# Kernel optimization log

Hardware: AMD Instinct MI355X
Metric: run time of the kernel (lower is better)

Reference implementation:

```python
import jax, jax.numpy as jnp
import numpy as np

TWO_PI = 2.0 * np.pi


def setup_inputs() -> dict:
    key = jax.random.key(0)
    k1, k2, k3, k4 = jax.random.split(key, 4)
    N, H, W, B = 1024, 256, 256, 64
    pred = jax.random.uniform(k1, (N,), dtype=jnp.float32)
    mu = jax.random.uniform(k2, (N, 2), dtype=jnp.float32)              # centers in [0,1]
    sigma = jax.random.uniform(k3, (N, 2), dtype=jnp.float32) * 0.25 + 0.05  # widths in [0.05,0.30]
    nodes = jnp.concatenate([mu, sigma], axis=1)                         # [N,4]
    batch_list = jax.random.randint(k4, (N,), 0, B, dtype=jnp.int64)
    return {"pred": pred, "nodes": nodes, "batch_list": batch_list,
            "h": H, "w": W, "batch_num": B}


def reference(pred, nodes, batch_list, h, w, batch_num):
    # Normalized grid, identical to torch.arange(num)*step + start
    xs = jnp.linspace(0.0, 1.0, w, dtype=pred.dtype)   # [w]
    ys = jnp.linspace(0.0, 1.0, h, dtype=pred.dtype)   # [h]
    x_t = xs[None, :]                                   # broadcasts to [h,w]
    y_t = ys[:, None]

    mu_x = nodes[:, 0][:, None, None]
    mu_y = nodes[:, 1][:, None, None]
    sx = nodes[:, 2][:, None, None]
    sy = nodes[:, 3][:, None, None]

    # [N,h,w] per-node gaussian (epsilon = 0 in the original module)
    g = (1.0 / (TWO_PI * sx * sy)) * jnp.exp(
        -((x_t[None] - mu_x) ** 2 / (2.0 * sx ** 2)
          + (y_t[None] - mu_y) ** 2 / (2.0 * sy ** 2)))

    # normalize each node map by its max, scale by pred[i]
    g = g / jnp.max(g, axis=(1, 2), keepdims=True) * pred[:, None, None]

    # scatter-add into per-batch maps
    maps = jax.ops.segment_sum(g, batch_list, num_segments=batch_num)   # [B,h,w]
    return maps[:, None, :, :]                                          # [B,1,h,w]
```

## Files before the change

### kernel.cpp

```cpp
#include <hip/hip_runtime.h>
#include <math.h>

#define HCONST 256
#define WCONST 256
#define ROWS   32
#define TILES  (HCONST / ROWS)
#define CHUNK  64

__global__ __launch_bounds__(256) void fused_kernel(
    const float* __restrict__ pred,
    const float* __restrict__ nodes,
    const int*   __restrict__ batch_list,
    int N,
    float* __restrict__ out)
{
    const int b  = blockIdx.x / TILES;
    const int ty = blockIdx.x % TILES;
    const int y0 = ty * ROWS;
    const int t  = threadIdx.x;
    const int xi   = t & 127;
    const int half = t >> 7;

    __shared__ int    s_idx[1024];
    __shared__ int    s_cnt;
    __shared__ float4 s_prm[CHUNK];
    __shared__ float  s_fy[CHUNK][ROWS];

    if (t == 0) s_cnt = 0;
    __syncthreads();
    for (int n = t; n < N; n += 256) {
        if (batch_list[n] == b) {
            int p = atomicAdd(&s_cnt, 1);
            s_idx[p] = n;
        }
    }
    __syncthreads();
    const int cnt = s_cnt;

    const float step = 1.0f / 255.0f;
    const float x0s = (2 * xi)     * step;
    const float x1s = (2 * xi + 1) * step;

    float2 acc[16];
#pragma unroll
    for (int r = 0; r < 16; ++r) acc[r] = make_float2(0.0f, 0.0f);

    for (int c0 = 0; c0 < cnt; c0 += CHUNK) {
        const int cc = min(CHUNK, cnt - c0);

        for (int p = t; p < cc; p += 256) {
            const int n = s_idx[c0 + p];
            const float4 nd = ((const float4*)nodes)[n];
            const float ax = 1.0f / (2.0f * nd.z * nd.z);
            float ni = roundf(nd.x * 255.0f);
            ni = fminf(fmaxf(ni, 0.0f), 255.0f);
            const float dxm = ni * step - nd.x;
            s_prm[p] = make_float4(nd.x, ax, ax * dxm * dxm, 0.0f);
        }
        for (int it = t; it < cc * ROWS; it += 256) {
            const int g  = it >> 5;
            const int yy = it & 31;
            const int n  = s_idx[c0 + g];
            const float4 nd = ((const float4*)nodes)[n];
            const float ay = 1.0f / (2.0f * nd.w * nd.w);
            float ni = roundf(nd.y * 255.0f);
            ni = fminf(fmaxf(ni, 0.0f), 255.0f);
            const float dym = ni * step - nd.y;
            const float dy  = (y0 + yy) * step - nd.y;
            s_fy[g][yy] = pred[n] * __expf(ay * (dym * dym - dy * dy));
        }
        __syncthreads();

        for (int g = 0; g < cc; ++g) {
            const float4 prm = s_prm[g];
            const float dx0 = x0s - prm.x;
            const float dx1 = x1s - prm.x;
            const float e0 = __expf(prm.z - prm.y * dx0 * dx0);
            const float e1 = __expf(prm.z - prm.y * dx1 * dx1);
            const float4* fy4 = (const float4*)&s_fy[g][half * 16];
#pragma unroll
            for (int k = 0; k < 4; ++k) {
                const float4 f = fy4[k];
                acc[k*4+0].x = fmaf(f.x, e0, acc[k*4+0].x);
                acc[k*4+0].y = fmaf(f.x, e1, acc[k*4+0].y);
                acc[k*4+1].x = fmaf(f.y, e0, acc[k*4+1].x);
                acc[k*4+1].y = fmaf(f.y, e1, acc[k*4+1].y);
                acc[k*4+2].x = fmaf(f.z, e0, acc[k*4+2].x);
                acc[k*4+2].y = fmaf(f.z, e1, acc[k*4+2].y);
                acc[k*4+3].x = fmaf(f.w, e0, acc[k*4+3].x);
                acc[k*4+3].y = fmaf(f.w, e1, acc[k*4+3].y);
            }
        }
        __syncthreads();
    }

    float* o = out + ((size_t)b * HCONST + y0 + half * 16) * WCONST + 2 * xi;
#pragma unroll
    for (int r = 0; r < 16; ++r)
        ((float2*)(o + (size_t)r * WCONST))[0] = acc[r];
}

extern "C" void kernel_launch(void* const* d_in, const int* in_sizes, int n_in,
                              void* d_out, int out_size, void* d_ws, size_t ws_size,
                              hipStream_t stream) {
    const float* pred       = (const float*)d_in[0];
    const float* nodes      = (const float*)d_in[1];
    const int*   batch_list = (const int*)d_in[2];

    const int N = in_sizes[0];
    const int B = out_size / (HCONST * WCONST);

    float* out = (float*)d_out;

    fused_kernel<<<B * TILES, 256, 0, stream>>>(pred, nodes, batch_list, N, out);
}
```

Measured before the change: 74.02 us.

## Halve row tile, vectorize batch scan, precompute y params, unroll node loop

Halves rows per block from 32 to 16, so the grid doubles to 1024 blocks with 8 accumulators per thread, and adds a launch-bounds occupancy hint. The batch_list scan now reads int4 vectors. Per-node x and y parameters, including pred, are computed once per node into shared memory, so the s_fy fill no longer reloads nodes and pred from global memory. The main accumulation loop processes two nodes per iteration. The cost is twice as many full scans of batch_list and more per-node exp work across blocks, since each block still evaluates the x exponentials for all of its nodes.

```diff
diff --git a/kernel.cpp b/kernel.cpp
--- a/kernel.cpp
+++ b/kernel.cpp
@@ -3,11 +3,11 @@
 
 #define HCONST 256
 #define WCONST 256
-#define ROWS   32
+#define ROWS   16
 #define TILES  (HCONST / ROWS)
 #define CHUNK  64
 
-__global__ __launch_bounds__(256) void fused_kernel(
+__global__ __launch_bounds__(256, 4) void fused_kernel(
     const float* __restrict__ pred,
     const float* __restrict__ nodes,
     const int*   __restrict__ batch_list,
@@ -23,16 +23,24 @@
 
     __shared__ int    s_idx[1024];
     __shared__ int    s_cnt;
-    __shared__ float4 s_prm[CHUNK];
+    __shared__ float4 s_px[CHUNK];
+    __shared__ float4 s_py[CHUNK];
     __shared__ float  s_fy[CHUNK][ROWS];
 
     if (t == 0) s_cnt = 0;
     __syncthreads();
-    for (int n = t; n < N; n += 256) {
-        if (batch_list[n] == b) {
-            int p = atomicAdd(&s_cnt, 1);
-            s_idx[p] = n;
+
+    {
+        const int4* bl4 = (const int4*)batch_list;
+        for (int q = t; q < (N >> 2); q += 256) {
+            const int4 v = bl4[q];
+            if (v.x == b) s_idx[atomicAdd(&s_cnt, 1)] = 4 * q;
+            if (v.y == b) s_idx[atomicAdd(&s_cnt, 1)] = 4 * q + 1;
+            if (v.z == b) s_idx[atomicAdd(&s_cnt, 1)] = 4 * q + 2;
+            if (v.w == b) s_idx[atomicAdd(&s_cnt, 1)] = 4 * q + 3;
         }
+        for (int n = (N & ~3) + t; n < N; n += 256)
+            if (batch_list[n] == b) s_idx[atomicAdd(&s_cnt, 1)] = n;
     }
     __syncthreads();
     const int cnt = s_cnt;
@@ -41,46 +49,80 @@
     const float x0s = (2 * xi)     * step;
     const float x1s = (2 * xi + 1) * step;
 
-    float2 acc[16];
+    float2 acc[8];
 #pragma unroll
-    for (int r = 0; r < 16; ++r) acc[r] = make_float2(0.0f, 0.0f);
+    for (int r = 0; r < 8; ++r) acc[r] = make_float2(0.0f, 0.0f);
 
     for (int c0 = 0; c0 < cnt; c0 += CHUNK) {
         const int cc = min(CHUNK, cnt - c0);
 
-        for (int p = t; p < cc; p += 256) {
-            const int n = s_idx[c0 + p];
+        if (t < cc) {
+            const int n = s_idx[c0 + t];
             const float4 nd = ((const float4*)nodes)[n];
+            const float pr = pred[n];
             const float ax = 1.0f / (2.0f * nd.z * nd.z);
-            float ni = roundf(nd.x * 255.0f);
-            ni = fminf(fmaxf(ni, 0.0f), 255.0f);
-            const float dxm = ni * step - nd.x;
-            s_prm[p] = make_float4(nd.x, ax, ax * dxm * dxm, 0.0f);
-        }
-        for (int it = t; it < cc * ROWS; it += 256) {
-            const int g  = it >> 5;
-            const int yy = it & 31;
-            const int n  = s_idx[c0 + g];
-            const float4 nd = ((const float4*)nodes)[n];
             const float ay = 1.0f / (2.0f * nd.w * nd.w);
-            float ni = roundf(nd.y * 255.0f);
-            ni = fminf(fmaxf(ni, 0.0f), 255.0f);
-            const float dym = ni * step - nd.y;
-            const float dy  = (y0 + yy) * step - nd.y;
-            s_fy[g][yy] = pred[n] * __expf(ay * (dym * dym - dy * dy));
+            float nix = fminf(fmaxf(roundf(nd.x * 255.0f), 0.0f), 255.0f);
+            float niy = fminf(fmaxf(roundf(nd.y * 255.0f), 0.0f), 255.0f);
+            const float dxm = nix * step - nd.x;
+            const float dym = niy * step - nd.y;
+            s_px[t] = make_float4(nd.x, ax, ax * dxm * dxm, 0.0f);
+            s_py[t] = make_float4(nd.y, ay, ay * dym * dym, pr);
         }
         __syncthreads();
 
-        for (int g = 0; g < cc; ++g) {
-            const float4 prm = s_prm[g];
-            const float dx0 = x0s - prm.x;
-            const float dx1 = x1s - prm.x;
-            const float e0 = __expf(prm.z - prm.y * dx0 * dx0);
-            const float e1 = __expf(prm.z - prm.y * dx1 * dx1);
-            const float4* fy4 = (const float4*)&s_fy[g][half * 16];
+        for (int it = t; it < cc * ROWS; it += 256) {
+            const int g  = it >> 4;
+            const int yy = it & 15;
+            const float4 py = s_py[g];
+            const float dy = (y0 + yy) * step - py.x;
+            s_fy[g][yy] = py.w * __expf(py.z - py.y * dy * dy);
+        }
+        __syncthreads();
+
+        int g = 0;
+        for (; g + 2 <= cc; g += 2) {
+            const float4 pa = s_px[g];
+            const float4 pb = s_px[g + 1];
+            const float dxa0 = x0s - pa.x, dxa1 = x1s - pa.x;
+            const float dxb0 = x0s - pb.x, dxb1 = x1s - pb.x;
+            const float ea0 = __expf(pa.z - pa.y * dxa0 * dxa0);
+            const float ea1 = __expf(pa.z - pa.y * dxa1 * dxa1);
+            const float eb0 = __expf(pb.z - pb.y * dxb0 * dxb0);
+            const float eb1 = __expf(pb.z - pb.y * dxb1 * dxb1);
+            const float4* fa4 = (const float4*)&s_fy[g][half * 8];
+            const float4* fb4 = (const float4*)&s_fy[g + 1][half * 8];
 #pragma unroll
-            for (int k = 0; k < 4; ++k) {
-                const float4 f = fy4[k];
+            for (int k = 0; k < 2; ++k) {
+                const float4 fa = fa4[k];
+                const float4 fb = fb4[k];
+                acc[k*4+0].x = fmaf(fa.x, ea0, acc[k*4+0].x);
+                acc[k*4+0].y = fmaf(fa.x, ea1, acc[k*4+0].y);
+                acc[k*4+1].x = fmaf(fa.y, ea0, acc[k*4+1].x);
+                acc[k*4+1].y = fmaf(fa.y, ea1, acc[k*4+1].y);
+                acc[k*4+2].x = fmaf(fa.z, ea0, acc[k*4+2].x);
+                acc[k*4+2].y = fmaf(fa.z, ea1, acc[k*4+2].y);
+                acc[k*4+3].x = fmaf(fa.w, ea0, acc[k*4+3].x);
+                acc[k*4+3].y = fmaf(fa.w, ea1, acc[k*4+3].y);
+                acc[k*4+0].x = fmaf(fb.x, eb0, acc[k*4+0].x);
+                acc[k*4+0].y = fmaf(fb.x, eb1, acc[k*4+0].y);
+                acc[k*4+1].x = fmaf(fb.y, eb0, acc[k*4+1].x);
+                acc[k*4+1].y = fmaf(fb.y, eb1, acc[k*4+1].y);
+                acc[k*4+2].x = fmaf(fb.z, eb0, acc[k*4+2].x);
+                acc[k*4+2].y = fmaf(fb.z, eb1, acc[k*4+2].y);
+                acc[k*4+3].x = fmaf(fb.w, eb0, acc[k*4+3].x);
+                acc[k*4+3].y = fmaf(fb.w, eb1, acc[k*4+3].y);
+            }
+        }
+        if (g < cc) {
+            const float4 pa = s_px[g];
+            const float dx0 = x0s - pa.x, dx1 = x1s - pa.x;
+            const float e0 = __expf(pa.z - pa.y * dx0 * dx0);
+            const float e1 = __expf(pa.z - pa.y * dx1 * dx1);
+            const float4* fa4 = (const float4*)&s_fy[g][half * 8];
+#pragma unroll
+            for (int k = 0; k < 2; ++k) {
+                const float4 f = fa4[k];
                 acc[k*4+0].x = fmaf(f.x, e0, acc[k*4+0].x);
                 acc[k*4+0].y = fmaf(f.x, e1, acc[k*4+0].y);
                 acc[k*4+1].x = fmaf(f.y, e0, acc[k*4+1].x);
@@ -94,9 +136,9 @@
         __syncthreads();
     }
 
-    float* o = out + ((size_t)b * HCONST + y0 + half * 16) * WCONST + 2 * xi;
+    float* o = out + ((size_t)b * HCONST + y0 + half * 8) * WCONST + 2 * xi;
 #pragma unroll
-    for (int r = 0; r < 16; ++r)
+    for (int r = 0; r < 8; ++r)
         ((float2*)(o + (size_t)r * WCONST))[0] = acc[r];
 }
 
```

Result: faster. 72.27 us (-2.4%).
